# Optimization experiments

Hardware: AMD Instinct MI355X
Metric: run time of the kernel (lower is better)

The kernel has to match this reference:

```python
import jax, jax.numpy as jnp
import numpy as np

B, N, M, C, H = 4, 2048, 2048, 1024, 16
D = C // H  # head_dim = 64
SCALE = D ** -0.5


def setup_inputs() -> dict:
    key = jax.random.key(0)
    ks = jax.random.split(key, 8)
    std = C ** -0.5
    return {
        "query": jax.random.normal(ks[0], (B, N, C), jnp.float32),
        "key": jax.random.normal(ks[1], (B, M, C), jnp.float32),
        "value": jax.random.normal(ks[2], (B, M, C), jnp.float32),
        "Wq": jax.random.normal(ks[3], (C, C), jnp.float32) * std,
        "Wk": jax.random.normal(ks[4], (C, C), jnp.float32) * std,
        "Wv": jax.random.normal(ks[5], (C, C), jnp.float32) * std,
        "Wp": jax.random.normal(ks[6], (C, C), jnp.float32) * std,
        "bp": jax.random.normal(ks[7], (C,), jnp.float32) * 0.01,
    }


def reference(query, key, value, Wq, Wk, Wv, Wp, bp):
    # Linear: y = x @ W.T (torch nn.Linear convention), no bias for q/k/v.
    # reshape (B,S,C)->(B,S,H,D)->(B,H,S,D)
    q = jnp.einsum('bnc,dc->bnd', query, Wq).reshape(B, N, H, D).transpose(0, 2, 1, 3)
    k = jnp.einsum('bmc,dc->bmd', key, Wk).reshape(B, M, H, D).transpose(0, 2, 1, 3)
    v = jnp.einsum('bmc,dc->bmd', value, Wv).reshape(B, M, H, D).transpose(0, 2, 1, 3)
    # scaled scores, softmax over keys
    attn = jnp.einsum('bhnd,bhmd->bhnm', q * SCALE, k)
    attn = jax.nn.softmax(attn, axis=-1)
    # attention output -> (B,N,C)
    x = jnp.einsum('bhnm,bhmd->bhnd', attn, v).transpose(0, 2, 1, 3).reshape(B, N, C)
    # output projection with bias
    return jnp.einsum('bnc,dc->bnd', x, Wp) + bp
```

## Files before the change

kernel.cpp:

```cpp
#include <hip/hip_runtime.h>
#include <stdint.h>

#define B_ 4
#define N_ 2048
#define M_ 2048
#define C_ 1024
#define H_ 16
#define D_ 64
#define SC_ (B_*N_*C_)
#define CC_ (C_*C_)

typedef unsigned short u16;
typedef __attribute__((ext_vector_type(8))) short short8;
typedef __attribute__((ext_vector_type(4))) float f32x4;

#if __has_builtin(__builtin_amdgcn_exp2f)
#define EXP2F __builtin_amdgcn_exp2f
#else
#define EXP2F exp2f
#endif

__device__ inline u16 f2bf(float f) {
    union { float f; uint32_t u; } v; v.f = f;
    uint32_t r = v.u + 0x7fffu + ((v.u >> 16) & 1u);
    return (u16)(r >> 16);
}

__global__ __launch_bounds__(256) void convert_kernel(
    const float* __restrict__ q, const float* __restrict__ k, const float* __restrict__ v,
    const float* __restrict__ wq, const float* __restrict__ wk,
    const float* __restrict__ wv, const float* __restrict__ wp,
    u16* __restrict__ qf, u16* __restrict__ kf, u16* __restrict__ vf,
    u16* __restrict__ wqb, u16* __restrict__ wkb, u16* __restrict__ wvb, u16* __restrict__ wpb)
{
    const int SC4 = SC_ / 4;
    const int CC4 = CC_ / 4;
    const int total = 3 * SC4 + 4 * CC4;
    for (int i = blockIdx.x * 256 + threadIdx.x; i < total; i += gridDim.x * 256) {
        const float* src; u16* dst; int off;
        if (i < 3 * SC4) {
            int seg = i >> 21;
            off = (i & (SC4 - 1)) << 2;
            src = seg == 0 ? q : seg == 1 ? k : v;
            dst = seg == 0 ? qf : seg == 1 ? kf : vf;
        } else {
            int j = i - 3 * SC4;
            int seg = j >> 18;
            off = (j & (CC4 - 1)) << 2;
            src = seg == 0 ? wq : seg == 1 ? wk : seg == 2 ? wv : wp;
            dst = seg == 0 ? wqb : seg == 1 ? wkb : seg == 2 ? wvb : wpb;
        }
        float4 val = *(const float4*)(src + off);
        ushort4 h;
        h.x = f2bf(val.x); h.y = f2bf(val.y); h.z = f2bf(val.z); h.w = f2bf(val.w);
        *(ushort4*)(dst + off) = h;
    }
}

template<int OMODE>
__global__ __launch_bounds__(256) void gemm_lds(
    const u16* __restrict__ A, const u16* __restrict__ Wb,
    const float* __restrict__ bias, void* __restrict__ Op, float scale)
{
    const int K = 1024;
    __shared__ u16 As[128 * 32];
    __shared__ u16 Bs[128 * 32];
    const int tid = threadIdx.x;
    const int wid = tid >> 6, lane = tid & 63;
    const int quad = lane >> 4, l15 = lane & 15;
    const int m0 = blockIdx.y * 128, n0 = blockIdx.x * 128;
    const int wm = (wid >> 1) * 64, wn = (wid & 1) * 64;

    f32x4 acc[4][4];
#pragma unroll
    for (int i = 0; i < 4; ++i)
#pragma unroll
        for (int j = 0; j < 4; ++j) acc[i][j] = f32x4{0.f, 0.f, 0.f, 0.f};

    for (int k0 = 0; k0 < K; k0 += 32) {
        __syncthreads();
#pragma unroll
        for (int i = 0; i < 2; ++i) {
            int s = tid + i * 256;
            int row = s >> 2, c8 = (s & 3) << 3;
            __builtin_amdgcn_global_load_lds(
                (const __attribute__((address_space(1))) void*)(A + (size_t)(m0 + row) * K + k0 + c8),
                (__attribute__((address_space(3))) void*)(As + s * 8), 16, 0, 0);
        }
#pragma unroll
        for (int i = 0; i < 2; ++i) {
            int s = tid + i * 256;
            int row = s >> 2, c8 = (s & 3) << 3;
            __builtin_amdgcn_global_load_lds(
                (const __attribute__((address_space(1))) void*)(Wb + (size_t)(n0 + row) * K + k0 + c8),
                (__attribute__((address_space(3))) void*)(Bs + s * 8), 16, 0, 0);
        }
        __syncthreads();

        short8 av[4], bv[4];
#pragma unroll
        for (int i = 0; i < 4; ++i)
            av[i] = *(const short8*)(As + (wm + i * 16 + l15) * 32 + quad * 8);
#pragma unroll
        for (int j = 0; j < 4; ++j)
            bv[j] = *(const short8*)(Bs + (wn + j * 16 + l15) * 32 + quad * 8);
#pragma unroll
        for (int i = 0; i < 4; ++i)
#pragma unroll
            for (int j = 0; j < 4; ++j)
                acc[i][j] = __builtin_amdgcn_mfma_f32_16x16x32_bf16(av[i], bv[j], acc[i][j], 0, 0, 0);
    }

    if (OMODE == 2) {
#pragma unroll
        for (int j = 0; j < 4; ++j) {
            int col = n0 + wn + j * 16 + l15;
            float bb = bias[col];
#pragma unroll
            for (int i = 0; i < 4; ++i) {
                int row = m0 + wm + i * 16 + quad * 4;
#pragma unroll
                for (int r = 0; r < 4; ++r)
                    ((float*)Op)[(size_t)(row + r) * 1024 + col] = acc[i][j][r] * scale + bb;
            }
        }
    } else if (OMODE == 0) {
#pragma unroll
        for (int j = 0; j < 4; ++j) {
            int col = n0 + wn + j * 16 + l15;
#pragma unroll
            for (int i = 0; i < 4; ++i) {
                int row = m0 + wm + i * 16 + quad * 4;
#pragma unroll
                for (int r = 0; r < 4; ++r)
                    ((u16*)Op)[(size_t)(row + r) * 1024 + col] = f2bf(acc[i][j][r] * scale);
            }
        }
    } else {
#pragma unroll
        for (int j = 0; j < 4; ++j) {
            int col = n0 + wn + j * 16 + l15;
            int hh = col >> 6, dd = col & 63;
#pragma unroll
            for (int i = 0; i < 4; ++i) {
                int row = m0 + wm + i * 16 + quad * 4;
                int bb = row >> 11, mm = row & 2047;
                ushort4 hv;
                hv.x = f2bf(acc[i][j][0] * scale);
                hv.y = f2bf(acc[i][j][1] * scale);
                hv.z = f2bf(acc[i][j][2] * scale);
                hv.w = f2bf(acc[i][j][3] * scale);
                *(ushort4*)((u16*)Op + (((size_t)bb * 16 + hh) * 64 + dd) * 2048 + mm) = hv;
            }
        }
    }
}

__global__ __launch_bounds__(256, 3) void attn_kernel(
    const u16* __restrict__ qg, const u16* __restrict__ kg,
    const u16* __restrict__ vT, u16* __restrict__ xb)
{
    __shared__ __align__(16) char smem[16384 + 4096];
    u16* Ks = (u16*)smem;
    u16* Vs = Ks + 4096;
    float* Ored = (float*)smem;
    float* Lred = (float*)(smem + 16384);

    const int tid = threadIdx.x;
    const int wid = tid >> 6, lane = tid & 63;
    const int quad = lane >> 4, l15 = lane & 15;
    const int b = blockIdx.z, h = blockIdx.y, qt = blockIdx.x;

    const u16* qbase = qg + ((size_t)(b * N_ + qt * 64)) * C_ + h * 64;
    short8 qf[4][2];
#pragma unroll
    for (int qb2 = 0; qb2 < 4; ++qb2)
#pragma unroll
        for (int ch = 0; ch < 2; ++ch)
            qf[qb2][ch] = *(const short8*)(qbase + (size_t)(qb2 * 16 + l15) * C_ + ch * 32 + quad * 8);

    const u16* kptr[2];
    const u16* vptr[2];
#pragma unroll
    for (int i = 0; i < 2; ++i) {
        int s = tid + i * 256;
        int row = s >> 3, g = s & 7;
        int gsw = g ^ (row & 7);
        kptr[i] = kg + ((size_t)(b * M_ + row)) * C_ + h * 64 + gsw * 8;
        vptr[i] = vT + (((size_t)b * 16 + h) * 64 + row) * M_ + gsw * 8;
    }

    f32x4 acc_o[4][4];
#pragma unroll
    for (int i = 0; i < 4; ++i)
#pragma unroll
        for (int j = 0; j < 4; ++j) acc_o[i][j] = f32x4{0.f, 0.f, 0.f, 0.f};
    float lsum[4] = {0.f, 0.f, 0.f, 0.f};

    const int rk = wid * 16 + l15, swk = rk & 7;
    const u16* kfp0 = Ks + rk * 64 + ((0 * 4 + quad) ^ swk) * 8;
    const u16* kfp1 = Ks + rk * 64 + ((1 * 4 + quad) ^ swk) * 8;
    const u16* vfp[4];
#pragma unroll
    for (int db = 0; db < 4; ++db) {
        int rv = db * 16 + l15, swv = rv & 7;
        vfp[db] = Vs + rv * 64 + (((wid * 2 + (quad >> 1)) ^ swv) << 3) + ((quad & 1) << 2);
    }

    for (int kv = 0; kv < M_; kv += 64) {
        __syncthreads();
#pragma unroll
        for (int i = 0; i < 2; ++i) {
            __builtin_amdgcn_global_load_lds(
                (const __attribute__((address_space(1))) void*)(kptr[i] + (size_t)kv * C_),
                (__attribute__((address_space(3))) void*)(Ks + (tid + i * 256) * 8), 16, 0, 0);
            __builtin_amdgcn_global_load_lds(
                (const __attribute__((address_space(1))) void*)(vptr[i] + kv),
                (__attribute__((address_space(3))) void*)(Vs + (tid + i * 256) * 8), 16, 0, 0);
        }
        __syncthreads();

        short8 kf0 = *(const short8*)kfp0;
        short8 kf1 = *(const short8*)kfp1;
        f32x4 sc[4];
#pragma unroll
        for (int qb2 = 0; qb2 < 4; ++qb2) {
            sc[qb2] = f32x4{0.f, 0.f, 0.f, 0.f};
            sc[qb2] = __builtin_amdgcn_mfma_f32_16x16x32_bf16(kf0, qf[qb2][0], sc[qb2], 0, 0, 0);
            sc[qb2] = __builtin_amdgcn_mfma_f32_16x16x32_bf16(kf1, qf[qb2][1], sc[qb2], 0, 0, 0);
        }

        union { short8 s; uint32_t u[4]; } pfrag[4];
#pragma unroll
        for (int qb2 = 0; qb2 < 4; ++qb2) {
            float e0 = EXP2F(sc[qb2][0]);
            float e1 = EXP2F(sc[qb2][1]);
            float e2 = EXP2F(sc[qb2][2]);
            float e3 = EXP2F(sc[qb2][3]);
            lsum[qb2] += (e0 + e1) + (e2 + e3);
            pfrag[qb2].u[0] = __builtin_amdgcn_perm(__builtin_bit_cast(uint32_t, e1),
                                                    __builtin_bit_cast(uint32_t, e0), 0x07060302u);
            pfrag[qb2].u[1] = __builtin_amdgcn_perm(__builtin_bit_cast(uint32_t, e3),
                                                    __builtin_bit_cast(uint32_t, e2), 0x07060302u);
            pfrag[qb2].u[2] = 0;
            pfrag[qb2].u[3] = 0;
        }

#pragma unroll
        for (int db = 0; db < 4; ++db) {
            uint2 vlo = *(const uint2*)vfp[db];
            union { short8 s; uint32_t u[4]; } vf;
            vf.u[0] = vlo.x; vf.u[1] = vlo.y; vf.u[2] = 0; vf.u[3] = 0;
#pragma unroll
            for (int qb2 = 0; qb2 < 4; ++qb2)
                acc_o[qb2][db] = __builtin_amdgcn_mfma_f32_16x16x32_bf16(vf.s, pfrag[qb2].s, acc_o[qb2][db], 0, 0, 0);
        }
    }

    __syncthreads();
    *(f32x4*)(Lred + (((wid * 4 + quad) * 16 + l15) << 2)) =
        f32x4{lsum[0], lsum[1], lsum[2], lsum[3]};
    __syncthreads();
    float dsum = 0.f;
#pragma unroll
    for (int q2 = 0; q2 < 4; ++q2)
        dsum += Lred[(((quad * 4 + q2) * 16 + l15) << 2) + wid];
    dsum += __shfl_xor(dsum, 16);
    dsum += __shfl_xor(dsum, 32);
    float dinv = 1.f / dsum;

#pragma unroll
    for (int qb2 = 0; qb2 < 4; ++qb2) {
        __syncthreads();
#pragma unroll
        for (int db = 0; db < 4; ++db)
            *(f32x4*)(Ored + (((wid * 4 + db) * 64 + lane) << 2)) = acc_o[qb2][db];
        __syncthreads();
        if (wid == qb2) {
#pragma unroll
            for (int w2 = 0; w2 < 4; ++w2) {
                if (w2 == wid) continue;
#pragma unroll
                for (int db = 0; db < 4; ++db) {
                    f32x4 t = *(const f32x4*)(Ored + (((w2 * 4 + db) * 64 + lane) << 2));
                    acc_o[qb2][db] += t;
                }
            }
            size_t ob = ((size_t)(b * N_ + qt * 64 + wid * 16 + l15)) * C_ + h * 64;
#pragma unroll
            for (int db = 0; db < 4; ++db) {
                ushort4 st;
                st.x = f2bf(acc_o[qb2][db][0] * dinv);
                st.y = f2bf(acc_o[qb2][db][1] * dinv);
                st.z = f2bf(acc_o[qb2][db][2] * dinv);
                st.w = f2bf(acc_o[qb2][db][3] * dinv);
                *(ushort4*)(xb + ob + db * 16 + quad * 4) = st;
            }
        }
    }
}

extern "C" void kernel_launch(void* const* d_in, const int* in_sizes, int n_in,
                              void* d_out, int out_size, void* d_ws, size_t ws_size,
                              hipStream_t stream) {
    const float* query = (const float*)d_in[0];
    const float* key   = (const float*)d_in[1];
    const float* value = (const float*)d_in[2];
    const float* Wq    = (const float*)d_in[3];
    const float* Wk    = (const float*)d_in[4];
    const float* Wv    = (const float*)d_in[5];
    const float* Wpm   = (const float*)d_in[6];
    const float* bp    = (const float*)d_in[7];
    float* out = (float*)d_out;

    u16* base = (u16*)d_ws;
    u16* qf  = base;
    u16* kf  = base + (size_t)SC_;
    u16* vf  = base + (size_t)2 * SC_;
    u16* kb  = base + (size_t)3 * SC_;
    u16* Wqb = base + (size_t)4 * SC_;
    u16* Wkb = Wqb + CC_;
    u16* Wvb = Wkb + CC_;
    u16* Wpb = Wvb + CC_;
    u16* vTp = kf;
    u16* qb  = vf;
    u16* xb  = qf;

    hipLaunchKernelGGL(convert_kernel, dim3(4096), dim3(256), 0, stream,
                       query, key, value, Wq, Wk, Wv, Wpm,
                       qf, kf, vf, Wqb, Wkb, Wvb, Wpb);

    dim3 gg(1024 / 128, (B_ * N_) / 128), bb(256);
    hipLaunchKernelGGL((gemm_lds<0>), gg, bb, 0, stream, kf, Wkb, nullptr, (void*)kb, 1.0f);
    hipLaunchKernelGGL((gemm_lds<1>), gg, bb, 0, stream, vf, Wvb, nullptr, (void*)vTp, 1.0f);
    hipLaunchKernelGGL((gemm_lds<0>), gg, bb, 0, stream, qf, Wqb, nullptr, (void*)qb,
                       0.125f * 1.44269504088896340736f);

    dim3 ga(N_ / 64, H_, B_);
    hipLaunchKernelGGL(attn_kernel, ga, bb, 0, stream, qb, kb, vTp, xb);

    hipLaunchKernelGGL((gemm_lds<2>), gg, bb, 0, stream, xb, Wpb, bp, (void*)out, 1.0f);
}
```

Before: 388.9 us.

## Double-buffer LDS tiles in GEMM and attention, remap grids to 1D

Both the projection GEMMs and the attention kernel now use two LDS buffers. The next K/V or A/W tile is prefetched with global_load_lds while the current tile is consumed, so each iteration needs one barrier instead of two and load latency can overlap with MFMA work. The launch grids become 1D with reordered block indices: GEMM walks M first, attention walks batch-head first. The attention kernel's launch bound rises to 4 blocks per CU. In exchange, LDS per block doubles, which may limit occupancy, and the new block order changes L2 reuse of K/V and weights.

Measured after the change: 441.8 us. 13.6% more time.

```diff
diff --git a/kernel.cpp b/kernel.cpp
--- a/kernel.cpp
+++ b/kernel.cpp
@@ -63,47 +63,64 @@
     const float* __restrict__ bias, void* __restrict__ Op, float scale)
 {
     const int K = 1024;
-    __shared__ u16 As[128 * 32];
-    __shared__ u16 Bs[128 * 32];
+    __shared__ u16 SH[2 * 8192];
     const int tid = threadIdx.x;
     const int wid = tid >> 6, lane = tid & 63;
     const int quad = lane >> 4, l15 = lane & 15;
-    const int m0 = blockIdx.y * 128, n0 = blockIdx.x * 128;
+    const int f = blockIdx.x;
+    const int m0 = (f & 63) * 128, n0 = (f >> 6) * 128;
     const int wm = (wid >> 1) * 64, wn = (wid & 1) * 64;
 
+    size_t aoff[2], boff[2];
+    int dsto[2];
+#pragma unroll
+    for (int i = 0; i < 2; ++i) {
+        int s = tid + i * 256;
+        int row = s >> 2, c8 = (s & 3) << 3;
+        aoff[i] = (size_t)(m0 + row) * K + c8;
+        boff[i] = (size_t)(n0 + row) * K + c8;
+        dsto[i] = s * 8;
+    }
+
     f32x4 acc[4][4];
 #pragma unroll
     for (int i = 0; i < 4; ++i)
 #pragma unroll
         for (int j = 0; j < 4; ++j) acc[i][j] = f32x4{0.f, 0.f, 0.f, 0.f};
 
-    for (int k0 = 0; k0 < K; k0 += 32) {
+#pragma unroll
+    for (int i = 0; i < 2; ++i) {
+        __builtin_amdgcn_global_load_lds(
+            (const __attribute__((address_space(1))) void*)(A + aoff[i]),
+            (__attribute__((address_space(3))) void*)(SH + dsto[i]), 16, 0, 0);
+        __builtin_amdgcn_global_load_lds(
+            (const __attribute__((address_space(1))) void*)(Wb + boff[i]),
+            (__attribute__((address_space(3))) void*)(SH + 4096 + dsto[i]), 16, 0, 0);
+    }
+
+    for (int it = 0; it < 32; ++it) {
+        const int cur = (it & 1) * 8192;
         __syncthreads();
-#pragma unroll
-        for (int i = 0; i < 2; ++i) {
-            int s = tid + i * 256;
-            int row = s >> 2, c8 = (s & 3) << 3;
-            __builtin_amdgcn_global_load_lds(
-                (const __attribute__((address_space(1))) void*)(A + (size_t)(m0 + row) * K + k0 + c8),
-                (__attribute__((address_space(3))) void*)(As + s * 8), 16, 0, 0);
-        }
-#pragma unroll
-        for (int i = 0; i < 2; ++i) {
-            int s = tid + i * 256;
-            int row = s >> 2, c8 = (s & 3) << 3;
-            __builtin_amdgcn_global_load_lds(
-                (const __attribute__((address_space(1))) void*)(Wb + (size_t)(n0 + row) * K + k0 + c8),
-                (__attribute__((address_space(3))) void*)(Bs + s * 8), 16, 0, 0);
-        }
-        __syncthreads();
-
+        if (it + 1 < 32) {
+            const int nxt = ((it + 1) & 1) * 8192;
+            const int k0n = (it + 1) * 32;
+#pragma unroll
+            for (int i = 0; i < 2; ++i) {
+                __builtin_amdgcn_global_load_lds(
+                    (const __attribute__((address_space(1))) void*)(A + aoff[i] + k0n),
+                    (__attribute__((address_space(3))) void*)(SH + nxt + dsto[i]), 16, 0, 0);
+                __builtin_amdgcn_global_load_lds(
+                    (const __attribute__((address_space(1))) void*)(Wb + boff[i] + k0n),
+                    (__attribute__((address_space(3))) void*)(SH + nxt + 4096 + dsto[i]), 16, 0, 0);
+            }
+        }
         short8 av[4], bv[4];
 #pragma unroll
         for (int i = 0; i < 4; ++i)
-            av[i] = *(const short8*)(As + (wm + i * 16 + l15) * 32 + quad * 8);
+            av[i] = *(const short8*)(SH + cur + (wm + i * 16 + l15) * 32 + quad * 8);
 #pragma unroll
         for (int j = 0; j < 4; ++j)
-            bv[j] = *(const short8*)(Bs + (wn + j * 16 + l15) * 32 + quad * 8);
+            bv[j] = *(const short8*)(SH + cur + 4096 + (wn + j * 16 + l15) * 32 + quad * 8);
 #pragma unroll
         for (int i = 0; i < 4; ++i)
 #pragma unroll
@@ -156,20 +173,21 @@
     }
 }
 
-__global__ __launch_bounds__(256, 3) void attn_kernel(
+__global__ __launch_bounds__(256, 4) void attn_kernel(
     const u16* __restrict__ qg, const u16* __restrict__ kg,
     const u16* __restrict__ vT, u16* __restrict__ xb)
 {
-    __shared__ __align__(16) char smem[16384 + 4096];
-    u16* Ks = (u16*)smem;
-    u16* Vs = Ks + 4096;
+    __shared__ __align__(16) char smem[32768 + 4096];
+    u16* KV = (u16*)smem;
     float* Ored = (float*)smem;
-    float* Lred = (float*)(smem + 16384);
+    float* Lred = (float*)(smem + 32768);
 
     const int tid = threadIdx.x;
     const int wid = tid >> 6, lane = tid & 63;
     const int quad = lane >> 4, l15 = lane & 15;
-    const int b = blockIdx.z, h = blockIdx.y, qt = blockIdx.x;
+    const int f = blockIdx.x;
+    const int bh = f & 63, qt = f >> 6;
+    const int b = bh >> 4, h = bh & 15;
 
     const u16* qbase = qg + ((size_t)(b * N_ + qt * 64)) * C_ + h * 64;
     short8 qf[4][2];
@@ -181,6 +199,7 @@
 
     const u16* kptr[2];
     const u16* vptr[2];
+    int dsto[2];
 #pragma unroll
     for (int i = 0; i < 2; ++i) {
         int s = tid + i * 256;
@@ -188,6 +207,7 @@
         int gsw = g ^ (row & 7);
         kptr[i] = kg + ((size_t)(b * M_ + row)) * C_ + h * 64 + gsw * 8;
         vptr[i] = vT + (((size_t)b * 16 + h) * 64 + row) * M_ + gsw * 8;
+        dsto[i] = s * 8;
     }
 
     f32x4 acc_o[4][4];
@@ -198,30 +218,49 @@
     float lsum[4] = {0.f, 0.f, 0.f, 0.f};
 
     const int rk = wid * 16 + l15, swk = rk & 7;
-    const u16* kfp0 = Ks + rk * 64 + ((0 * 4 + quad) ^ swk) * 8;
-    const u16* kfp1 = Ks + rk * 64 + ((1 * 4 + quad) ^ swk) * 8;
-    const u16* vfp[4];
+    const int kfo0 = rk * 64 + ((0 * 4 + quad) ^ swk) * 8;
+    const int kfo1 = rk * 64 + ((1 * 4 + quad) ^ swk) * 8;
+    int vfo[4];
 #pragma unroll
     for (int db = 0; db < 4; ++db) {
         int rv = db * 16 + l15, swv = rv & 7;
-        vfp[db] = Vs + rv * 64 + (((wid * 2 + (quad >> 1)) ^ swv) << 3) + ((quad & 1) << 2);
-    }
-
-    for (int kv = 0; kv < M_; kv += 64) {
+        vfo[db] = 4096 + rv * 64 + (((wid * 2 + (quad >> 1)) ^ swv) << 3) + ((quad & 1) << 2);
+    }
+
+    union { short8 s; uint32_t u[4]; } pfrag[4], vfu;
+#pragma unroll
+    for (int qb2 = 0; qb2 < 4; ++qb2) { pfrag[qb2].u[2] = 0; pfrag[qb2].u[3] = 0; }
+    vfu.u[2] = 0; vfu.u[3] = 0;
+
+#pragma unroll
+    for (int i = 0; i < 2; ++i) {
+        __builtin_amdgcn_global_load_lds(
+            (const __attribute__((address_space(1))) void*)(kptr[i]),
+            (__attribute__((address_space(3))) void*)(KV + dsto[i]), 16, 0, 0);
+        __builtin_amdgcn_global_load_lds(
+            (const __attribute__((address_space(1))) void*)(vptr[i]),
+            (__attribute__((address_space(3))) void*)(KV + 4096 + dsto[i]), 16, 0, 0);
+    }
+
+    for (int it = 0; it < 32; ++it) {
+        const int cur = (it & 1) * 8192;
         __syncthreads();
-#pragma unroll
-        for (int i = 0; i < 2; ++i) {
-            __builtin_amdgcn_global_load_lds(
-                (const __attribute__((address_space(1))) void*)(kptr[i] + (size_t)kv * C_),
-                (__attribute__((address_space(3))) void*)(Ks + (tid + i * 256) * 8), 16, 0, 0);
-            __builtin_amdgcn_global_load_lds(
-                (const __attribute__((address_space(1))) void*)(vptr[i] + kv),
-                (__attribute__((address_space(3))) void*)(Vs + (tid + i * 256) * 8), 16, 0, 0);
-        }
-        __syncthreads();
-
-        short8 kf0 = *(const short8*)kfp0;
-        short8 kf1 = *(const short8*)kfp1;
+        if (it + 1 < 32) {
+            const int nxt = ((it + 1) & 1) * 8192;
+            const int kvn = (it + 1) * 64;
+#pragma unroll
+            for (int i = 0; i < 2; ++i) {
+                __builtin_amdgcn_global_load_lds(
+                    (const __attribute__((address_space(1))) void*)(kptr[i] + (size_t)kvn * C_),
+                    (__attribute__((address_space(3))) void*)(KV + nxt + dsto[i]), 16, 0, 0);
+                __builtin_amdgcn_global_load_lds(
+                    (const __attribute__((address_space(1))) void*)(vptr[i] + kvn),
+                    (__attribute__((address_space(3))) void*)(KV + nxt + 4096 + dsto[i]), 16, 0, 0);
+            }
+        }
+
+        short8 kf0 = *(const short8*)(KV + cur + kfo0);
+        short8 kf1 = *(const short8*)(KV + cur + kfo1);
         f32x4 sc[4];
 #pragma unroll
         for (int qb2 = 0; qb2 < 4; ++qb2) {
@@ -230,7 +269,6 @@
             sc[qb2] = __builtin_amdgcn_mfma_f32_16x16x32_bf16(kf1, qf[qb2][1], sc[qb2], 0, 0, 0);
         }
 
-        union { short8 s; uint32_t u[4]; } pfrag[4];
 #pragma unroll
         for (int qb2 = 0; qb2 < 4; ++qb2) {
             float e0 = EXP2F(sc[qb2][0]);
@@ -242,18 +280,15 @@
                                                     __builtin_bit_cast(uint32_t, e0), 0x07060302u);
             pfrag[qb2].u[1] = __builtin_amdgcn_perm(__builtin_bit_cast(uint32_t, e3),
                                                     __builtin_bit_cast(uint32_t, e2), 0x07060302u);
-            pfrag[qb2].u[2] = 0;
-            pfrag[qb2].u[3] = 0;
         }
 
 #pragma unroll
         for (int db = 0; db < 4; ++db) {
-            uint2 vlo = *(const uint2*)vfp[db];
-            union { short8 s; uint32_t u[4]; } vf;
-            vf.u[0] = vlo.x; vf.u[1] = vlo.y; vf.u[2] = 0; vf.u[3] = 0;
+            uint2 vlo = *(const uint2*)(KV + cur + vfo[db]);
+            vfu.u[0] = vlo.x; vfu.u[1] = vlo.y;
 #pragma unroll
             for (int qb2 = 0; qb2 < 4; ++qb2)
-                acc_o[qb2][db] = __builtin_amdgcn_mfma_f32_16x16x32_bf16(vf.s, pfrag[qb2].s, acc_o[qb2][db], 0, 0, 0);
+                acc_o[qb2][db] = __builtin_amdgcn_mfma_f32_16x16x32_bf16(vfu.s, pfrag[qb2].s, acc_o[qb2][db], 0, 0, 0);
         }
     }
 
@@ -330,14 +365,13 @@
                        query, key, value, Wq, Wk, Wv, Wpm,
                        qf, kf, vf, Wqb, Wkb, Wvb, Wpb);
 
-    dim3 gg(1024 / 128, (B_ * N_) / 128), bb(256);
+    dim3 gg(512), bb(256);
     hipLaunchKernelGGL((gemm_lds<0>), gg, bb, 0, stream, kf, Wkb, nullptr, (void*)kb, 1.0f);
     hipLaunchKernelGGL((gemm_lds<1>), gg, bb, 0, stream, vf, Wvb, nullptr, (void*)vTp, 1.0f);
     hipLaunchKernelGGL((gemm_lds<0>), gg, bb, 0, stream, qf, Wqb, nullptr, (void*)qb,
                        0.125f * 1.44269504088896340736f);
 
-    dim3 ga(N_ / 64, H_, B_);
-    hipLaunchKernelGGL(attn_kernel, ga, bb, 0, stream, qb, kb, vTp, xb);
+    hipLaunchKernelGGL(attn_kernel, dim3(2048), bb, 0, stream, qb, kb, vTp, xb);
 
     hipLaunchKernelGGL((gemm_lds<2>), gg, bb, 0, stream, xb, Wpb, bp, (void*)out, 1.0f);
 }
```
